# Performance work log

Hardware: AMD Instinct MI355X
Metric: run time of the kernel (lower is better)

## Reference

```python
import jax, jax.numpy as jnp
import numpy as np

B, T, E, H = 8, 2048, 1024, 64

def setup_inputs() -> dict:
    key = jax.random.key(0)
    k1, k2, k3, k4 = jax.random.split(key, 4)
    x = jax.random.normal(k1, (B, T, E), dtype=jnp.float32)
    # match nn.Linear init scale roughly (values only affect numerics, not math)
    s = 1.0 / np.sqrt(E)
    Wk = jax.random.normal(k2, (E, H), dtype=jnp.float32) * s
    Wq = jax.random.normal(k3, (E, H), dtype=jnp.float32) * s
    Wv = jax.random.normal(k4, (E, H), dtype=jnp.float32) * s
    return {"x": x, "Wk": Wk, "Wq": Wq, "Wv": Wv}

def reference(x, Wk, Wq, Wv):
    # projections: [B,T,E] @ [E,H] -> [B,T,H]
    k = x @ Wk
    q = x @ Wq
    v = x @ Wv
    scale = k.shape[-1] ** -0.5
    # scores [B,T,T]
    scores = jnp.einsum('bth,bsh->bts', q, k) * scale
    Tq = x.shape[1]
    causal = jnp.tril(jnp.ones((Tq, Tq), dtype=bool))
    scores = jnp.where(causal, scores, -jnp.inf)
    weights = jax.nn.softmax(scores, axis=-1)
    # dropout p=0.0 -> identity
    att = jnp.einsum('bts,bsh->bth', weights, v)  # [B,T,H]
    return att
```

## Files before the change

kernel.cpp:

```cpp
#include <hip/hip_runtime.h>
#include <hip/hip_bf16.h>

typedef _Float16 f16;
typedef _Float16 f16x8 __attribute__((ext_vector_type(8)));
typedef float f32x4 __attribute__((ext_vector_type(4)));

#define NB 8
#define NT 2048
#define NE 1024
#define NH 64

#define CHUNKS_PER_BATCH 144
#define MAXC 8

#define OFF_WT 0
#define OFF_QH 393216
#define OFF_KH 2490368
#define OFF_VT 4587520
#define OFF_ML 6684672
#define OFF_OP 7733248

__global__ __launch_bounds__(256) void wconv_kernel(
        const float* __restrict__ Wk, const float* __restrict__ Wq,
        const float* __restrict__ Wv, f16* __restrict__ wt) {
    __shared__ float tile[64][65];
    const int mat = blockIdx.x >> 4;
    const int e0 = (blockIdx.x & 15) * 64;
    const float* W = (mat == 0) ? Wq : (mat == 1) ? Wk : Wv;
    const int tx = threadIdx.x & 63;
    const int ty = threadIdx.x >> 6;
#pragma unroll
    for (int r = ty; r < 64; r += 4)
        tile[r][tx] = W[(size_t)(e0 + r) * NH + tx];
    __syncthreads();
#pragma unroll
    for (int h = ty; h < 64; h += 4)
        wt[(size_t)mat * (NH * NE) + (size_t)h * NE + e0 + tx] = (f16)tile[tx][h];
}

__global__ __launch_bounds__(256) void qkv_proj_kernel(
        const float* __restrict__ x, const f16* __restrict__ wt,
        f16* __restrict__ Qh, f16* __restrict__ Kh, f16* __restrict__ VT) {
    __shared__ f16 xs[2][64 * 64];
    __shared__ f16 wsb[2][192 * 64];

    const int tid = threadIdx.x;
    const int wave = tid >> 6;
    const int lane = tid & 63;
    const int lr = lane & 15;
    const int lg = lane >> 4;
    const int m0 = blockIdx.x * 64;
    const int nt0 = wave * 3;

    f32x4 acc[12] = {};

    float4 xr0, xr1, xr2, xr3;
    int4 wr0, wr1, wr2, wr3, wr4, wr5;

    const int xrow = tid >> 2;
    const int xcg = (tid & 3) * 16;

#define ISSUE_LOADS(kc)                                                        \
    do {                                                                       \
        const float* xb = x + (size_t)(m0 + xrow) * NE + (kc) + xcg;           \
        xr0 = *(const float4*)(xb);                                            \
        xr1 = *(const float4*)(xb + 4);                                        \
        xr2 = *(const float4*)(xb + 8);                                        \
        xr3 = *(const float4*)(xb + 12);                                       \
        wr0 = *(const int4*)(wt + (size_t)((tid + 0 * 256) >> 3) * NE + (kc) + ((tid + 0 * 256) & 7) * 8); \
        wr1 = *(const int4*)(wt + (size_t)((tid + 1 * 256) >> 3) * NE + (kc) + ((tid + 1 * 256) & 7) * 8); \
        wr2 = *(const int4*)(wt + (size_t)((tid + 2 * 256) >> 3) * NE + (kc) + ((tid + 2 * 256) & 7) * 8); \
        wr3 = *(const int4*)(wt + (size_t)((tid + 3 * 256) >> 3) * NE + (kc) + ((tid + 3 * 256) & 7) * 8); \
        wr4 = *(const int4*)(wt + (size_t)((tid + 4 * 256) >> 3) * NE + (kc) + ((tid + 4 * 256) & 7) * 8); \
        wr5 = *(const int4*)(wt + (size_t)((tid + 5 * 256) >> 3) * NE + (kc) + ((tid + 5 * 256) & 7) * 8); \
    } while (0)

#define CVT8(dst, a0, a1)                                                      \
    f16x8 dst = { (f16)a0.x, (f16)a0.y, (f16)a0.z, (f16)a0.w,                  \
                  (f16)a1.x, (f16)a1.y, (f16)a1.z, (f16)a1.w }

#define WRITE_LDS(buf)                                                         \
    do {                                                                       \
        { CVT8(v0, xr0, xr1);                                                  \
          int c = (tid & 3) * 2;                                               \
          int byo = xrow * 128 + ((c * 16) ^ ((xrow & 7) << 4));               \
          *(f16x8*)((char*)xs[buf] + byo) = v0; }                              \
        { CVT8(v1, xr2, xr3);                                                  \
          int c = (tid & 3) * 2 + 1;                                           \
          int byo = xrow * 128 + ((c * 16) ^ ((xrow & 7) << 4));               \
          *(f16x8*)((char*)xs[buf] + byo) = v1; }                              \
        { int jw = tid + 0 * 256, n = jw >> 3, c = jw & 7;                     \
          *(int4*)((char*)wsb[buf] + n * 128 + ((c * 16) ^ ((n & 7) << 4))) = wr0; } \
        { int jw = tid + 1 * 256, n = jw >> 3, c = jw & 7;                     \
          *(int4*)((char*)wsb[buf] + n * 128 + ((c * 16) ^ ((n & 7) << 4))) = wr1; } \
        { int jw = tid + 2 * 256, n = jw >> 3, c = jw & 7;                     \
          *(int4*)((char*)wsb[buf] + n * 128 + ((c * 16) ^ ((n & 7) << 4))) = wr2; } \
        { int jw = tid + 3 * 256, n = jw >> 3, c = jw & 7;                     \
          *(int4*)((char*)wsb[buf] + n * 128 + ((c * 16) ^ ((n & 7) << 4))) = wr3; } \
        { int jw = tid + 4 * 256, n = jw >> 3, c = jw & 7;                     \
          *(int4*)((char*)wsb[buf] + n * 128 + ((c * 16) ^ ((n & 7) << 4))) = wr4; } \
        { int jw = tid + 5 * 256, n = jw >> 3, c = jw & 7;                     \
          *(int4*)((char*)wsb[buf] + n * 128 + ((c * 16) ^ ((n & 7) << 4))) = wr5; } \
    } while (0)

    ISSUE_LOADS(0);
    WRITE_LDS(0);
    __syncthreads();

    int cur = 0;
    for (int c = 0; c < 16; ++c) {
        if (c < 15) ISSUE_LOADS((c + 1) * 64);

#pragma unroll
        for (int ks = 0; ks < 2; ++ks) {
            f16x8 af[4], bf[3];
#pragma unroll
            for (int mt = 0; mt < 4; ++mt) {
                int row = mt * 16 + lr;
                int byo = row * 128 + ((ks * 64 + lg * 16) ^ ((row & 7) << 4));
                af[mt] = *(const f16x8*)((const char*)xs[cur] + byo);
            }
#pragma unroll
            for (int j = 0; j < 3; ++j) {
                int n = (nt0 + j) * 16 + lr;
                int byo = n * 128 + ((ks * 64 + lg * 16) ^ ((n & 7) << 4));
                bf[j] = *(const f16x8*)((const char*)wsb[cur] + byo);
            }
#pragma unroll
            for (int mt = 0; mt < 4; ++mt)
#pragma unroll
                for (int j = 0; j < 3; ++j)
                    acc[mt * 3 + j] = __builtin_amdgcn_mfma_f32_16x16x32_f16(
                        af[mt], bf[j], acc[mt * 3 + j], 0, 0, 0);
        }

        __syncthreads();
        if (c < 15) {
            WRITE_LDS(cur ^ 1);
            __syncthreads();
        }
        cur ^= 1;
    }

#pragma unroll
    for (int j = 0; j < 3; ++j) {
        int nbase = (nt0 + j) * 16;
        int mat = nbase >> 6;
        int ncol = (nbase & 63) + lr;
#pragma unroll
        for (int mt = 0; mt < 4; ++mt) {
#pragma unroll
            for (int r = 0; r < 4; ++r) {
                int m = m0 + mt * 16 + lg * 4 + r;
                f16 val = (f16)acc[mt * 3 + j][r];
                if (mat == 0) {
                    Qh[(size_t)m * NH + ncol] = val;
                } else if (mat == 1) {
                    Kh[(size_t)m * NH + ncol] = val;
                } else {
                    int bb = m >> 11;
                    int tt = m & 2047;
                    VT[((size_t)bb * NH + ncol) * NT + tt] = val;
                }
            }
        }
    }
#undef ISSUE_LOADS
#undef CVT8
#undef WRITE_LDS
}

__global__ __launch_bounds__(256) void attn_part_kernel(
        const f16* __restrict__ Qh, const f16* __restrict__ Kh,
        const f16* __restrict__ VT, f16* __restrict__ op, float2* __restrict__ ml) {
    __shared__ f16 pbuf[4][16][40];

    const int wave = threadIdx.x >> 6;
    const int lane = threadIdx.x & 63;
    const int lr = lane & 15;
    const int lg = lane >> 4;

    const int b = blockIdx.x / CHUNKS_PER_BATCH;
    int c = blockIdx.x % CHUNKS_PER_BATCH;
    int qi = 0;
    for (; qi < 32; ++qi) {
        int ncq = (qi + 4) >> 2;
        if (c < ncq) break;
        c -= ncq;
    }
    const int total_steps = (qi + 1) * 2;
    const int sbeg = c * 8;
    const int send = min(sbeg + 8, total_steps);
    const int qbase = qi * 64;
    const int qrow = qbase + wave * 16;

    const f16* Qb = Qh + (size_t)b * NT * NH;
    const f16* Kb = Kh + (size_t)b * NT * NH;
    const f16* Vb = VT + (size_t)b * NH * NT;

    f16x8 qf[2];
#pragma unroll
    for (int h = 0; h < 2; ++h)
        qf[h] = *(const f16x8*)(Qb + (size_t)(qrow + lr) * NH + h * 32 + lg * 8);

    f32x4 o[4] = {};
    float mrow[4], lrow[4];
#pragma unroll
    for (int r = 0; r < 4; ++r) { mrow[r] = -INFINITY; lrow[r] = 0.f; }

    const float scale = 0.125f;

    for (int s = sbeg; s < send; ++s) {
        const int s0 = s * 32;

        f32x4 S[2] = {};
#pragma unroll
        for (int t = 0; t < 2; ++t) {
#pragma unroll
            for (int h = 0; h < 2; ++h) {
                f16x8 kf = *(const f16x8*)(Kb + (size_t)(s0 + t * 16 + lr) * NH + h * 32 + lg * 8);
                S[t] = __builtin_amdgcn_mfma_f32_16x16x32_f16(qf[h], kf, S[t], 0, 0, 0);
            }
        }

#pragma unroll
        for (int t = 0; t < 2; ++t) {
#pragma unroll
            for (int r = 0; r < 4; ++r) {
                int q = qrow + lg * 4 + r;
                int key = s0 + t * 16 + lr;
                float sv = S[t][r] * scale;
                S[t][r] = (key <= q) ? sv : -INFINITY;
            }
        }

        float mx[4];
#pragma unroll
        for (int r = 0; r < 4; ++r) mx[r] = fmaxf(S[0][r], S[1][r]);
#pragma unroll
        for (int d = 1; d < 16; d <<= 1) {
#pragma unroll
            for (int r = 0; r < 4; ++r) mx[r] = fmaxf(mx[r], __shfl_xor(mx[r], d));
        }

        float f[4], nms[4];
#pragma unroll
        for (int r = 0; r < 4; ++r) {
            float nm = fmaxf(mrow[r], mx[r]);
            nms[r] = (nm == -INFINITY) ? 0.f : nm;
            f[r] = __expf(mrow[r] - nms[r]);
            mrow[r] = nm;
        }

#pragma unroll
        for (int t = 0; t < 2; ++t) {
#pragma unroll
            for (int r = 0; r < 4; ++r) S[t][r] = __expf(S[t][r] - nms[r]);
        }

#pragma unroll
        for (int r = 0; r < 4; ++r) {
            float rsum = S[0][r] + S[1][r];
#pragma unroll
            for (int d = 1; d < 16; d <<= 1) rsum += __shfl_xor(rsum, d);
            lrow[r] = lrow[r] * f[r] + rsum;
        }

#pragma unroll
        for (int ht = 0; ht < 4; ++ht) {
#pragma unroll
            for (int r = 0; r < 4; ++r) o[ht][r] *= f[r];
        }

#pragma unroll
        for (int t = 0; t < 2; ++t) {
#pragma unroll
            for (int r = 0; r < 4; ++r)
                pbuf[wave][lg * 4 + r][t * 16 + lr] = (f16)S[t][r];
        }
        __builtin_amdgcn_wave_barrier();
        f16x8 pf = *(const f16x8*)(&pbuf[wave][lr][lg * 8]);

#pragma unroll
        for (int ht = 0; ht < 4; ++ht) {
            f16x8 vf = *(const f16x8*)(Vb + (size_t)(ht * 16 + lr) * NT + s0 + lg * 8);
            o[ht] = __builtin_amdgcn_mfma_f32_16x16x32_f16(pf, vf, o[ht], 0, 0, 0);
        }
        __builtin_amdgcn_wave_barrier();
    }

#pragma unroll
    for (int r = 0; r < 4; ++r) {
        int qt = qrow + lg * 4 + r;
        size_t slot = ((size_t)b * NT + qt) * MAXC + c;
#pragma unroll
        for (int ht = 0; ht < 4; ++ht)
            op[slot * NH + ht * 16 + lr] = (f16)o[ht][r];
        if (lr == 0) {
            float2 v; v.x = mrow[r]; v.y = lrow[r];
            ml[slot] = v;
        }
    }
}

__global__ __launch_bounds__(256) void combine_kernel(
        const f16* __restrict__ op, const float2* __restrict__ ml,
        float* __restrict__ out) {
    int gid = blockIdx.x * 256 + threadIdx.x;
    int row = gid >> 6;
    int h = gid & 63;
    int q = row & (NT - 1);
    int qi = q >> 6;
    int nc = (qi + 4) >> 2;

    size_t base = (size_t)row * MAXC;
    float2 ml0 = ml[base];
    float M = ml0.x, L = ml0.y;
    float O = (float)op[base * NH + h];
    for (int cc = 1; cc < nc; ++cc) {
        float2 mlc = ml[base + cc];
        if (mlc.x == -INFINITY) continue;
        float oc = (float)op[(base + cc) * NH + h];
        float nM = fmaxf(M, mlc.x);
        float wo = __expf(M - nM), wc = __expf(mlc.x - nM);
        O = O * wo + oc * wc;
        L = L * wo + mlc.y * wc;
        M = nM;
    }
    out[gid] = O / L;
}

extern "C" void kernel_launch(void* const* d_in, const int* in_sizes, int n_in,
                              void* d_out, int out_size, void* d_ws, size_t ws_size,
                              hipStream_t stream) {
    const float* x  = (const float*)d_in[0];
    const float* Wk = (const float*)d_in[1];
    const float* Wq = (const float*)d_in[2];
    const float* Wv = (const float*)d_in[3];
    float* out = (float*)d_out;

    char* ws = (char*)d_ws;
    f16* wt    = (f16*)(ws + OFF_WT);
    f16* Qh    = (f16*)(ws + OFF_QH);
    f16* Kh    = (f16*)(ws + OFF_KH);
    f16* VT    = (f16*)(ws + OFF_VT);
    float2* ml = (float2*)(ws + OFF_ML);
    f16* op    = (f16*)(ws + OFF_OP);

    hipLaunchKernelGGL(wconv_kernel, dim3(48), dim3(256), 0, stream, Wk, Wq, Wv, wt);
    hipLaunchKernelGGL(qkv_proj_kernel, dim3(256), dim3(256), 0, stream, x, wt, Qh, Kh, VT);
    hipLaunchKernelGGL(attn_part_kernel, dim3(NB * CHUNKS_PER_BATCH), dim3(256), 0, stream,
                       Qh, Kh, VT, op, ml);
    hipLaunchKernelGGL(combine_kernel, dim3(NB * NT * NH / 256), dim3(256), 0, stream,
                       op, ml, out);
}
```

Baseline: 173.7 us.

## Process 64 keys per iteration, fold scale into Q, skip masking and rescale

Each loop iteration now handles 64 keys instead of 32, doubling the MFMA work between softmax reductions. The 1/sqrt(H) scale is folded into the Q fragment once. Causal masking runs only for tiles that touch the diagonal, and the rescale of O and l is skipped when no row's max grew (checked with a wave ballot). This cuts per-key ALU and shuffle overhead. Prescaling Q in fp16 slightly changes numerics, and the step range must stay even for the 2-step loop to be correct.

```diff
diff --git a/kernel.cpp b/kernel.cpp
--- a/kernel.cpp
+++ b/kernel.cpp
@@ -173,7 +173,7 @@
 __global__ __launch_bounds__(256) void attn_part_kernel(
         const f16* __restrict__ Qh, const f16* __restrict__ Kh,
         const f16* __restrict__ VT, f16* __restrict__ op, float2* __restrict__ ml) {
-    __shared__ f16 pbuf[4][16][40];
+    __shared__ f16 pbuf[4][16][72];
 
     const int wave = threadIdx.x >> 6;
     const int lane = threadIdx.x & 63;
@@ -200,22 +200,23 @@
 
     f16x8 qf[2];
 #pragma unroll
-    for (int h = 0; h < 2; ++h)
+    for (int h = 0; h < 2; ++h) {
         qf[h] = *(const f16x8*)(Qb + (size_t)(qrow + lr) * NH + h * 32 + lg * 8);
+#pragma unroll
+        for (int j = 0; j < 8; ++j) qf[h][j] = qf[h][j] * (f16)0.125f;
+    }
 
     f32x4 o[4] = {};
     float mrow[4], lrow[4];
 #pragma unroll
     for (int r = 0; r < 4; ++r) { mrow[r] = -INFINITY; lrow[r] = 0.f; }
 
-    const float scale = 0.125f;
-
-    for (int s = sbeg; s < send; ++s) {
-        const int s0 = s * 32;
-
-        f32x4 S[2] = {};
-#pragma unroll
-        for (int t = 0; t < 2; ++t) {
+    for (int s2 = sbeg; s2 < send; s2 += 2) {
+        const int s0 = s2 * 32;
+
+        f32x4 S[4] = {};
+#pragma unroll
+        for (int t = 0; t < 4; ++t) {
 #pragma unroll
             for (int h = 0; h < 2; ++h) {
                 f16x8 kf = *(const f16x8*)(Kb + (size_t)(s0 + t * 16 + lr) * NH + h * 32 + lg * 8);
@@ -223,68 +224,77 @@
             }
         }
 
-#pragma unroll
-        for (int t = 0; t < 2; ++t) {
+        if (s0 + 63 > qrow) {
+#pragma unroll
+            for (int t = 0; t < 4; ++t) {
+#pragma unroll
+                for (int r = 0; r < 4; ++r) {
+                    int q = qrow + lg * 4 + r;
+                    int key = s0 + t * 16 + lr;
+                    S[t][r] = (key <= q) ? S[t][r] : -INFINITY;
+                }
+            }
+        }
+
+        float mx[4];
+#pragma unroll
+        for (int r = 0; r < 4; ++r)
+            mx[r] = fmaxf(fmaxf(S[0][r], S[1][r]), fmaxf(S[2][r], S[3][r]));
+#pragma unroll
+        for (int d = 1; d < 16; d <<= 1) {
+#pragma unroll
+            for (int r = 0; r < 4; ++r) mx[r] = fmaxf(mx[r], __shfl_xor(mx[r], d));
+        }
+
+        float nms[4];
+        bool grow = false;
+#pragma unroll
+        for (int r = 0; r < 4; ++r) grow = grow || (mx[r] > mrow[r]);
+        if (__ballot(grow) != 0ull) {
 #pragma unroll
             for (int r = 0; r < 4; ++r) {
-                int q = qrow + lg * 4 + r;
-                int key = s0 + t * 16 + lr;
-                float sv = S[t][r] * scale;
-                S[t][r] = (key <= q) ? sv : -INFINITY;
-            }
-        }
-
-        float mx[4];
-#pragma unroll
-        for (int r = 0; r < 4; ++r) mx[r] = fmaxf(S[0][r], S[1][r]);
-#pragma unroll
-        for (int d = 1; d < 16; d <<= 1) {
-#pragma unroll
-            for (int r = 0; r < 4; ++r) mx[r] = fmaxf(mx[r], __shfl_xor(mx[r], d));
-        }
-
-        float f[4], nms[4];
+                float nm = fmaxf(mrow[r], mx[r]);
+                nms[r] = (nm == -INFINITY) ? 0.f : nm;
+                float fr = __expf(mrow[r] - nms[r]);
+                mrow[r] = nm;
+                lrow[r] *= fr;
+#pragma unroll
+                for (int ht = 0; ht < 4; ++ht) o[ht][r] *= fr;
+            }
+        } else {
+#pragma unroll
+            for (int r = 0; r < 4; ++r) nms[r] = (mrow[r] == -INFINITY) ? 0.f : mrow[r];
+        }
+
+#pragma unroll
+        for (int t = 0; t < 4; ++t) {
+#pragma unroll
+            for (int r = 0; r < 4; ++r) S[t][r] = __expf(S[t][r] - nms[r]);
+        }
 #pragma unroll
         for (int r = 0; r < 4; ++r) {
-            float nm = fmaxf(mrow[r], mx[r]);
-            nms[r] = (nm == -INFINITY) ? 0.f : nm;
-            f[r] = __expf(mrow[r] - nms[r]);
-            mrow[r] = nm;
-        }
-
-#pragma unroll
-        for (int t = 0; t < 2; ++t) {
-#pragma unroll
-            for (int r = 0; r < 4; ++r) S[t][r] = __expf(S[t][r] - nms[r]);
-        }
-
-#pragma unroll
-        for (int r = 0; r < 4; ++r) {
-            float rsum = S[0][r] + S[1][r];
+            float rsum = (S[0][r] + S[1][r]) + (S[2][r] + S[3][r]);
 #pragma unroll
             for (int d = 1; d < 16; d <<= 1) rsum += __shfl_xor(rsum, d);
-            lrow[r] = lrow[r] * f[r] + rsum;
-        }
-
-#pragma unroll
-        for (int ht = 0; ht < 4; ++ht) {
-#pragma unroll
-            for (int r = 0; r < 4; ++r) o[ht][r] *= f[r];
-        }
-
-#pragma unroll
-        for (int t = 0; t < 2; ++t) {
+            lrow[r] += rsum;
+        }
+
+#pragma unroll
+        for (int t = 0; t < 4; ++t) {
 #pragma unroll
             for (int r = 0; r < 4; ++r)
                 pbuf[wave][lg * 4 + r][t * 16 + lr] = (f16)S[t][r];
         }
         __builtin_amdgcn_wave_barrier();
-        f16x8 pf = *(const f16x8*)(&pbuf[wave][lr][lg * 8]);
+        f16x8 pf0 = *(const f16x8*)(&pbuf[wave][lr][lg * 8]);
+        f16x8 pf1 = *(const f16x8*)(&pbuf[wave][lr][32 + lg * 8]);
 
 #pragma unroll
         for (int ht = 0; ht < 4; ++ht) {
-            f16x8 vf = *(const f16x8*)(Vb + (size_t)(ht * 16 + lr) * NT + s0 + lg * 8);
-            o[ht] = __builtin_amdgcn_mfma_f32_16x16x32_f16(pf, vf, o[ht], 0, 0, 0);
+            f16x8 vf0 = *(const f16x8*)(Vb + (size_t)(ht * 16 + lr) * NT + s0 + lg * 8);
+            f16x8 vf1 = *(const f16x8*)(Vb + (size_t)(ht * 16 + lr) * NT + s0 + 32 + lg * 8);
+            o[ht] = __builtin_amdgcn_mfma_f32_16x16x32_f16(pf0, vf0, o[ht], 0, 0, 0);
+            o[ht] = __builtin_amdgcn_mfma_f32_16x16x32_f16(pf1, vf1, o[ht], 0, 0, 0);
         }
         __builtin_amdgcn_wave_barrier();
     }
```

Result: no change. 175.5 us (+1.0%).

## Widen attention key step to 64 with double-buffered K prefetch and lazy rescale

Applied to the files above, without the earlier changes.

The attention partial kernel now processes 64 keys per iteration instead of 32, prefetches the next K tile into alternating register buffers while computing the current one, and loads V before the score computation. The softmax scale is folded into Q once, the causal mask is applied only on diagonal tiles, and the running-max rescale of the output and denominator is skipped when no row max grows in the wave. This aims to hide global load latency and cut per-step ALU and exp work, at the cost of more registers (which may lower occupancy) and the assumption that the 8-step chunk boundaries stay even.

```diff
diff --git a/kernel.cpp b/kernel.cpp
--- a/kernel.cpp
+++ b/kernel.cpp
@@ -173,7 +173,7 @@
 __global__ __launch_bounds__(256) void attn_part_kernel(
         const f16* __restrict__ Qh, const f16* __restrict__ Kh,
         const f16* __restrict__ VT, f16* __restrict__ op, float2* __restrict__ ml) {
-    __shared__ f16 pbuf[4][16][40];
+    __shared__ f16 pbuf[4][16][72];
 
     const int wave = threadIdx.x >> 6;
     const int lane = threadIdx.x & 63;
@@ -200,94 +200,143 @@
 
     f16x8 qf[2];
 #pragma unroll
-    for (int h = 0; h < 2; ++h)
+    for (int h = 0; h < 2; ++h) {
         qf[h] = *(const f16x8*)(Qb + (size_t)(qrow + lr) * NH + h * 32 + lg * 8);
+#pragma unroll
+        for (int j = 0; j < 8; ++j) qf[h][j] = qf[h][j] * (f16)0.125f;
+    }
 
     f32x4 o[4] = {};
     float mrow[4], lrow[4];
 #pragma unroll
     for (int r = 0; r < 4; ++r) { mrow[r] = -INFINITY; lrow[r] = 0.f; }
 
-    const float scale = 0.125f;
-
-    for (int s = sbeg; s < send; ++s) {
-        const int s0 = s * 32;
-
-        f32x4 S[2] = {};
-#pragma unroll
-        for (int t = 0; t < 2; ++t) {
-#pragma unroll
-            for (int h = 0; h < 2; ++h) {
-                f16x8 kf = *(const f16x8*)(Kb + (size_t)(s0 + t * 16 + lr) * NH + h * 32 + lg * 8);
-                S[t] = __builtin_amdgcn_mfma_f32_16x16x32_f16(qf[h], kf, S[t], 0, 0, 0);
-            }
-        }
-
-#pragma unroll
-        for (int t = 0; t < 2; ++t) {
-#pragma unroll
-            for (int r = 0; r < 4; ++r) {
-                int q = qrow + lg * 4 + r;
-                int key = s0 + t * 16 + lr;
-                float sv = S[t][r] * scale;
-                S[t][r] = (key <= q) ? sv : -INFINITY;
-            }
-        }
-
-        float mx[4];
-#pragma unroll
-        for (int r = 0; r < 4; ++r) mx[r] = fmaxf(S[0][r], S[1][r]);
-#pragma unroll
-        for (int d = 1; d < 16; d <<= 1) {
-#pragma unroll
-            for (int r = 0; r < 4; ++r) mx[r] = fmaxf(mx[r], __shfl_xor(mx[r], d));
-        }
-
-        float f[4], nms[4];
-#pragma unroll
-        for (int r = 0; r < 4; ++r) {
-            float nm = fmaxf(mrow[r], mx[r]);
-            nms[r] = (nm == -INFINITY) ? 0.f : nm;
-            f[r] = __expf(mrow[r] - nms[r]);
-            mrow[r] = nm;
-        }
-
-#pragma unroll
-        for (int t = 0; t < 2; ++t) {
-#pragma unroll
-            for (int r = 0; r < 4; ++r) S[t][r] = __expf(S[t][r] - nms[r]);
-        }
-
-#pragma unroll
-        for (int r = 0; r < 4; ++r) {
-            float rsum = S[0][r] + S[1][r];
-#pragma unroll
-            for (int d = 1; d < 16; d <<= 1) rsum += __shfl_xor(rsum, d);
-            lrow[r] = lrow[r] * f[r] + rsum;
-        }
-
-#pragma unroll
-        for (int ht = 0; ht < 4; ++ht) {
-#pragma unroll
-            for (int r = 0; r < 4; ++r) o[ht][r] *= f[r];
-        }
-
-#pragma unroll
-        for (int t = 0; t < 2; ++t) {
-#pragma unroll
-            for (int r = 0; r < 4; ++r)
-                pbuf[wave][lg * 4 + r][t * 16 + lr] = (f16)S[t][r];
-        }
-        __builtin_amdgcn_wave_barrier();
-        f16x8 pf = *(const f16x8*)(&pbuf[wave][lr][lg * 8]);
-
-#pragma unroll
-        for (int ht = 0; ht < 4; ++ht) {
-            f16x8 vf = *(const f16x8*)(Vb + (size_t)(ht * 16 + lr) * NT + s0 + lg * 8);
-            o[ht] = __builtin_amdgcn_mfma_f32_16x16x32_f16(pf, vf, o[ht], 0, 0, 0);
-        }
-        __builtin_amdgcn_wave_barrier();
-    }
+    f16x8 kfA[8], kfB[8], vf[8];
+
+#define ISSUE_K(KARR, s0_)                                                     \
+    do {                                                                       \
+        _Pragma("unroll")                                                      \
+        for (int t = 0; t < 4; ++t) {                                          \
+            _Pragma("unroll")                                                  \
+            for (int h = 0; h < 2; ++h)                                        \
+                KARR[t * 2 + h] = *(const f16x8*)(                             \
+                    Kb + (size_t)((s0_) + t * 16 + lr) * NH + h * 32 + lg * 8);\
+        }                                                                      \
+    } while (0)
+
+#define ISSUE_V(s0_)                                                           \
+    do {                                                                       \
+        _Pragma("unroll")                                                      \
+        for (int t = 0; t < 4; ++t) {                                          \
+            vf[t * 2 + 0] = *(const f16x8*)(                                   \
+                Vb + (size_t)(t * 16 + lr) * NT + (s0_) + lg * 8);             \
+            vf[t * 2 + 1] = *(const f16x8*)(                                   \
+                Vb + (size_t)(t * 16 + lr) * NT + (s0_) + 32 + lg * 8);        \
+        }                                                                      \
+    } while (0)
+
+#define STEP_COMPUTE(KARR, s0_)                                                \
+    do {                                                                       \
+        f32x4 S[4] = {};                                                       \
+        _Pragma("unroll")                                                      \
+        for (int t = 0; t < 4; ++t) {                                          \
+            _Pragma("unroll")                                                  \
+            for (int h = 0; h < 2; ++h)                                        \
+                S[t] = __builtin_amdgcn_mfma_f32_16x16x32_f16(                 \
+                    qf[h], KARR[t * 2 + h], S[t], 0, 0, 0);                    \
+        }                                                                      \
+        if ((s0_) + 63 > qrow) {                                               \
+            _Pragma("unroll")                                                  \
+            for (int t = 0; t < 4; ++t) {                                      \
+                _Pragma("unroll")                                              \
+                for (int r = 0; r < 4; ++r) {                                  \
+                    int q = qrow + lg * 4 + r;                                 \
+                    int key = (s0_) + t * 16 + lr;                             \
+                    S[t][r] = (key <= q) ? S[t][r] : -INFINITY;                \
+                }                                                              \
+            }                                                                  \
+        }                                                                      \
+        float mx[4];                                                           \
+        _Pragma("unroll")                                                      \
+        for (int r = 0; r < 4; ++r)                                            \
+            mx[r] = fmaxf(fmaxf(S[0][r], S[1][r]), fmaxf(S[2][r], S[3][r]));   \
+        _Pragma("unroll")                                                      \
+        for (int d = 1; d < 16; d <<= 1) {                                     \
+            _Pragma("unroll")                                                  \
+            for (int r = 0; r < 4; ++r) mx[r] = fmaxf(mx[r], __shfl_xor(mx[r], d)); \
+        }                                                                      \
+        float nms[4];                                                          \
+        bool grow = false;                                                     \
+        _Pragma("unroll")                                                      \
+        for (int r = 0; r < 4; ++r) grow = grow || (mx[r] > mrow[r]);          \
+        if (__ballot(grow) != 0ull) {                                          \
+            _Pragma("unroll")                                                  \
+            for (int r = 0; r < 4; ++r) {                                      \
+                float nm = fmaxf(mrow[r], mx[r]);                              \
+                nms[r] = (nm == -INFINITY) ? 0.f : nm;                         \
+                float fr = __expf(mrow[r] - nms[r]);                           \
+                mrow[r] = nm;                                                  \
+                lrow[r] *= fr;                                                 \
+                _Pragma("unroll")                                              \
+                for (int ht = 0; ht < 4; ++ht) o[ht][r] *= fr;                 \
+            }                                                                  \
+        } else {                                                               \
+            _Pragma("unroll")                                                  \
+            for (int r = 0; r < 4; ++r)                                        \
+                nms[r] = (mrow[r] == -INFINITY) ? 0.f : mrow[r];               \
+        }                                                                      \
+        _Pragma("unroll")                                                      \
+        for (int t = 0; t < 4; ++t) {                                          \
+            _Pragma("unroll")                                                  \
+            for (int r = 0; r < 4; ++r) S[t][r] = __expf(S[t][r] - nms[r]);    \
+        }                                                                      \
+        _Pragma("unroll")                                                      \
+        for (int r = 0; r < 4; ++r) {                                          \
+            float rsum = (S[0][r] + S[1][r]) + (S[2][r] + S[3][r]);            \
+            _Pragma("unroll")                                                  \
+            for (int d = 1; d < 16; d <<= 1) rsum += __shfl_xor(rsum, d);      \
+            lrow[r] += rsum;                                                   \
+        }                                                                      \
+        _Pragma("unroll")                                                      \
+        for (int t = 0; t < 4; ++t) {                                          \
+            _Pragma("unroll")                                                  \
+            for (int r = 0; r < 4; ++r)                                        \
+                pbuf[wave][lg * 4 + r][t * 16 + lr] = (f16)S[t][r];            \
+        }                                                                      \
+        __builtin_amdgcn_wave_barrier();                                       \
+        f16x8 pf0 = *(const f16x8*)(&pbuf[wave][lr][lg * 8]);                  \
+        f16x8 pf1 = *(const f16x8*)(&pbuf[wave][lr][32 + lg * 8]);             \
+        _Pragma("unroll")                                                      \
+        for (int ht = 0; ht < 4; ++ht) {                                       \
+            o[ht] = __builtin_amdgcn_mfma_f32_16x16x32_f16(pf0, vf[ht * 2 + 0], o[ht], 0, 0, 0); \
+            o[ht] = __builtin_amdgcn_mfma_f32_16x16x32_f16(pf1, vf[ht * 2 + 1], o[ht], 0, 0, 0); \
+        }                                                                      \
+        __builtin_amdgcn_wave_barrier();                                       \
+    } while (0)
+
+    int s2 = sbeg;
+    ISSUE_K(kfA, s2 * 32);
+    for (;;) {
+        {
+            const int s0 = s2 * 32;
+            ISSUE_V(s0);
+            if (s2 + 2 < send) ISSUE_K(kfB, (s2 + 2) * 32);
+            STEP_COMPUTE(kfA, s0);
+            s2 += 2;
+            if (s2 >= send) break;
+        }
+        {
+            const int s0 = s2 * 32;
+            ISSUE_V(s0);
+            if (s2 + 2 < send) ISSUE_K(kfA, (s2 + 2) * 32);
+            STEP_COMPUTE(kfB, s0);
+            s2 += 2;
+            if (s2 >= send) break;
+        }
+    }
+#undef ISSUE_K
+#undef ISSUE_V
+#undef STEP_COMPUTE
 
 #pragma unroll
     for (int r = 0; r < 4; ++r) {
```

Measured after the change: 171.3 us. About the same (-1.4%).
